# Performance work log

Hardware: AMD Instinct MI355X
Metric: run time of the kernel (lower is better)

## Reference

```python
import jax, jax.numpy as jnp
import numpy as np
from jax import lax

K = 8192
D = 256
BETA = 0.1
DECAY = 0.99
EPS = 1e-05


def setup_inputs() -> dict:
    key = jax.random.key(0)
    k1, k2, k3 = jax.random.split(key, 3)
    z_e = jax.random.normal(k1, (8, 2048, D), dtype=jnp.float32)
    codebook = jax.random.normal(k2, (K, D), dtype=jnp.float32)
    ema_cluster_size = jnp.zeros((K,), dtype=jnp.float32)
    ema_w = jax.random.normal(k3, (K, D), dtype=jnp.float32)
    return {"z_e": z_e, "codebook": codebook,
            "ema_cluster_size": ema_cluster_size, "ema_w": ema_w}


def reference(z_e, codebook, ema_cluster_size, ema_w):
    B, L, Dd = z_e.shape
    # squared-distance matrix (B, L, K): ||z||^2 - 2 z.C^T + ||c||^2
    dist = ((z_e ** 2).sum(-1, keepdims=True)
            - 2.0 * jnp.einsum('bld,kd->blk', z_e, codebook)
            + (codebook ** 2).sum(-1))
    codes = jnp.argmin(dist, axis=-1)          # (B, L) int
    z_q = codebook[codes]                      # gather (B, L, D)

    # training-mode EMA statistics (segment_sum == one_hot.T @ z_e, memory-light)
    flat_codes = codes.reshape(-1)
    flat_z = z_e.reshape(-1, Dd)
    n_i = jax.ops.segment_sum(jnp.ones(flat_codes.shape, dtype=z_e.dtype),
                              flat_codes, num_segments=K)
    dw = jax.ops.segment_sum(flat_z, flat_codes, num_segments=K)
    new_cluster_size = DECAY * ema_cluster_size + (1.0 - DECAY) * n_i
    new_ema_w = DECAY * ema_w + (1.0 - DECAY) * dw
    new_codebook = new_ema_w / (new_cluster_size + EPS)[:, None]

    # straight-through combine and commitment loss
    z_q_st = z_e + lax.stop_gradient(z_q - z_e)
    vq_loss = BETA * jnp.mean((z_e - lax.stop_gradient(z_q)) ** 2)
    return z_q_st, codes, vq_loss, new_codebook, new_cluster_size, new_ema_w
```

## Files before the change

### kernel.cpp

```cpp
#include <hip/hip_runtime.h>
#include <hip/hip_bf16.h>
#include <math.h>

#define N_ROWS 16384
#define DIM    256
#define KCODES 8192

#define OFF_ZQ    0
#define OFF_CODES 4194304
#define OFF_LOSS  4210688
#define OFF_CB    4210689
#define OFF_CS    6307841
#define OFF_EW    6316033
#define OUT_TOTAL 8413185

typedef __attribute__((ext_vector_type(8))) short bf16x8;
typedef __attribute__((ext_vector_type(4))) float f32x4;
typedef __attribute__((ext_vector_type(16))) float f32x16;

__device__ __forceinline__ void gll16(const void* g, void* l) {
  __builtin_amdgcn_global_load_lds(
      (const __attribute__((address_space(1))) unsigned int*)g,
      (__attribute__((address_space(3))) unsigned int*)l, 16, 0, 0);
}

__device__ __forceinline__ unsigned short f2bf(float x) {
  __hip_bfloat16 h = __float2bfloat16(x);
  return *reinterpret_cast<unsigned short*>(&h);
}

__device__ __forceinline__ unsigned umin32(unsigned a, unsigned b) { return a < b ? a : b; }
__device__ __forceinline__ unsigned umax32(unsigned a, unsigned b) { return a > b ? a : b; }

__global__ __launch_bounds__(256) void k_pre(
    const float* __restrict__ z, unsigned short* __restrict__ zbuf,
    const float* __restrict__ cb, unsigned short* __restrict__ cbt,
    float* __restrict__ cnormb, int* __restrict__ cnt,
    float* __restrict__ loss_part) {
  const int b = blockIdx.x;
  const int tid = threadIdx.x;
  if (b < 2048) {
    int i = b * 256 + tid;
    const float4 a = ((const float4*)z)[i * 2];
    const float4 c = ((const float4*)z)[i * 2 + 1];
    union { unsigned short u[8]; uint4 v; } o;
    o.u[0] = f2bf(a.x); o.u[1] = f2bf(a.y); o.u[2] = f2bf(a.z); o.u[3] = f2bf(a.w);
    o.u[4] = f2bf(c.x); o.u[5] = f2bf(c.y); o.u[6] = f2bf(c.z); o.u[7] = f2bf(c.w);
    ((uint4*)zbuf)[i] = o.v;
  } else if (b < 3072) {
    const int code = (b - 2048) * 8 + (tid >> 5);
    const int dq = tid & 31;
    const float4 v0 = *(const float4*)(cb + (size_t)code * 256 + dq * 8);
    const float4 v1 = *(const float4*)(cb + (size_t)code * 256 + dq * 8 + 4);
    union { unsigned short u[8]; uint4 q; } o;
    o.u[0] = f2bf(-2.f * v0.x); o.u[1] = f2bf(-2.f * v0.y);
    o.u[2] = f2bf(-2.f * v0.z); o.u[3] = f2bf(-2.f * v0.w);
    o.u[4] = f2bf(-2.f * v1.x); o.u[5] = f2bf(-2.f * v1.y);
    o.u[6] = f2bf(-2.f * v1.z); o.u[7] = f2bf(-2.f * v1.w);
    *(uint4*)(cbt + ((size_t)dq * 8192 + code) * 8) = o.q;
    float s = v0.x * v0.x + v0.y * v0.y + v0.z * v0.z + v0.w * v0.w +
              v1.x * v1.x + v1.y * v1.y + v1.z * v1.z + v1.w * v1.w;
#pragma unroll
    for (int off = 16; off >= 1; off >>= 1) s += __shfl_down(s, off);
    if ((tid & 31) == 0) cnormb[code] = s + 1024.0f;
  } else if (cnt) {
    int zi = (b - 3072) * 256 + tid;
    if (zi < 8192) cnt[zi] = 0;
    else if (zi < 8448) loss_part[zi - 8192] = 0.0f;
  }
}

__global__ __launch_bounds__(256, 2) void k_argmin(
    const unsigned short* __restrict__ zb,
    const unsigned short* __restrict__ cbt,
    const float* __restrict__ cnb,
    unsigned long long* __restrict__ partials) {
  __shared__ __align__(16) unsigned char lds[73728];

  const int tid = threadIdx.x;
  const int lane = tid & 63;
  const int w = tid >> 6;
  const int wc = w & 1;
  const int wr = w >> 1;
  const int hi = lane >> 5;
  const int l31 = lane & 31;
  const int chunk = blockIdx.x;
  const int r0 = blockIdx.y << 7;

  {
    const char* zgb = (const char*)zb + (size_t)r0 * 512;
#pragma unroll
    for (int it = 0; it < 16; ++it) {
      int s = it * 256 + tid;
      int row = s >> 5;
      int dql = (tid & 31) ^ (row & 31);
      gll16(zgb + row * 512 + dql * 16, lds + s * 16);
    }
    gll16((const char*)cnb + (size_t)chunk * 8192 + tid * 16,
          lds + 65536 + tid * 16);
    gll16((const char*)cnb + (size_t)chunk * 8192 + 4096 + tid * 16,
          lds + 69632 + tid * 16);
  }
  asm volatile("s_waitcnt vmcnt(0)" ::: "memory");
  __builtin_amdgcn_s_barrier();
  __builtin_amdgcn_sched_barrier(0);

  bf16x8 zr0[16], zr1[16];
  {
    const int xr = l31 * 16;
    const int rb0 = (wr * 64 + l31) * 512;
    const int rb1 = (wr * 64 + 32 + l31) * 512;
    const int hx = hi * 16;
#pragma unroll
    for (int ks = 0; ks < 16; ++ks) {
      zr0[ks] = *(const bf16x8*)(lds + rb0 + ((ks * 32 + hx) ^ xr));
      zr1[ks] = *(const bf16x8*)(lds + rb1 + ((ks * 32 + hx) ^ xr));
    }
  }
  asm volatile("s_waitcnt lgkmcnt(0)" ::: "memory");
  __builtin_amdgcn_s_barrier();
  __builtin_amdgcn_sched_barrier(0);

  unsigned char* lcb = lds + tid * 16;
  const char* cgc = (const char*)cbt +
      ((size_t)(tid >> 7) * 131072 + (size_t)chunk * 32768 + (tid & 127) * 16);
  gll16(cgc + 0 * 262144, lcb + 0 * 4096);
  gll16(cgc + 1 * 262144, lcb + 1 * 4096);
  gll16(cgc + 2 * 262144, lcb + 2 * 4096);

  const unsigned char* afp = lds + hi * 2048 + (wc * 64 + l31) * 16;
  const unsigned wchi4 = (unsigned)(wc * 64 + hi * 4);

  unsigned k1_00 = 0xFFFFFFFFu, k2_00 = 0xFFFFFFFFu;
  unsigned k1_01 = 0xFFFFFFFFu, k2_01 = 0xFFFFFFFFu;
  unsigned k1_10 = 0xFFFFFFFFu, k2_10 = 0xFFFFFFFFu;
  unsigned k1_11 = 0xFFFFFFFFu, k2_11 = 0xFFFFFFFFu;
  f32x16 acc00, acc01, acc10, acc11;

#define KSTEP(ks, TAIL)                                                        \
  {                                                                            \
    if ((TAIL) && (ks) == 14) asm volatile("s_waitcnt vmcnt(1)" ::: "memory"); \
    else if ((TAIL) && (ks) == 15) asm volatile("s_waitcnt vmcnt(0)" ::: "memory"); \
    else asm volatile("s_waitcnt vmcnt(2)" ::: "memory");                      \
    __builtin_amdgcn_s_barrier();                                              \
    __builtin_amdgcn_sched_barrier(0);                                         \
    if ((ks) < 13) {                                                           \
      gll16(cgc + ((ks) + 3) * 262144, lcb + (((ks) + 3) & 3) * 4096);         \
    } else if (!(TAIL)) {                                                      \
      gll16(cgc + 2048 + ((ks) - 13) * 262144, lcb + (((ks) + 3) & 3) * 4096); \
    }                                                                          \
    bf16x8 a0 = *(const bf16x8*)(afp + ((ks) & 3) * 4096);                     \
    bf16x8 a1 = *(const bf16x8*)(afp + ((ks) & 3) * 4096 + 512);               \
    acc00 = __builtin_amdgcn_mfma_f32_32x32x16_bf16(a0, zr0[ks], acc00, 0, 0, 0); \
    acc01 = __builtin_amdgcn_mfma_f32_32x32x16_bf16(a0, zr1[ks], acc01, 0, 0, 0); \
    acc10 = __builtin_amdgcn_mfma_f32_32x32x16_bf16(a1, zr0[ks], acc10, 0, 0, 0); \
    acc11 = __builtin_amdgcn_mfma_f32_32x32x16_bf16(a1, zr1[ks], acc11, 0, 0, 0); \
  }

#define MRG(K1V, K2V, KEY)                                                     \
  {                                                                            \
    unsigned t_ = umax32(K1V, (KEY));                                          \
    K2V = umin32(K2V, t_);                                                     \
    K1V = umin32(K1V, (KEY));                                                  \
  }

#define CTBODY(HALF, TAIL)                                                     \
  {                                                                            \
    const int cnoff = 65536 + (HALF) * 4096 + ct * 512 + wc * 256 + hi * 16;   \
    f32x4 cnA[4], cnB[4];                                                      \
    _Pragma("unroll") for (int g2 = 0; g2 < 4; ++g2) {                         \
      cnA[g2] = *(const f32x4*)(lds + cnoff + g2 * 32);                        \
      cnB[g2] = *(const f32x4*)(lds + cnoff + 128 + g2 * 32);                  \
    }                                                                          \
    _Pragma("unroll") for (int r = 0; r < 16; ++r) {                           \
      float vA = cnA[r >> 2][r & 3], vB = cnB[r >> 2][r & 3];                  \
      acc00[r] = vA; acc01[r] = vA; acc10[r] = vB; acc11[r] = vB;              \
    }                                                                          \
    KSTEP(0, TAIL)  KSTEP(1, TAIL)  KSTEP(2, TAIL)  KSTEP(3, TAIL)             \
    KSTEP(4, TAIL)  KSTEP(5, TAIL)  KSTEP(6, TAIL)  KSTEP(7, TAIL)             \
    KSTEP(8, TAIL)  KSTEP(9, TAIL)  KSTEP(10, TAIL) KSTEP(11, TAIL)            \
    KSTEP(12, TAIL) KSTEP(13, TAIL) KSTEP(14, TAIL) KSTEP(15, TAIL)            \
    const unsigned vb = (unsigned)(ct * 128) | wchi4;                          \
    _Pragma("unroll") for (int r = 0; r < 16; ++r) {                           \
      const unsigned base = (unsigned)(8 * (r >> 2) + (r & 3));                \
      unsigned key;                                                            \
      key = (__float_as_uint(acc00[r]) & 0xFFFFFC00u) | (vb | base);           \
      MRG(k1_00, k2_00, key)                                                   \
      key = (__float_as_uint(acc01[r]) & 0xFFFFFC00u) | (vb | base);           \
      MRG(k1_01, k2_01, key)                                                   \
      key = (__float_as_uint(acc10[r]) & 0xFFFFFC00u) | (vb | base | 32u);     \
      MRG(k1_10, k2_10, key)                                                   \
      key = (__float_as_uint(acc11[r]) & 0xFFFFFC00u) | (vb | base | 32u);     \
      MRG(k1_11, k2_11, key)                                                   \
    }                                                                          \
    cgc += 2048;                                                               \
  }

  for (int ct = 0; ct < 8; ++ct) CTBODY(0, false)
  unsigned s1_00 = k1_00, s2_00 = k2_00, s1_01 = k1_01, s2_01 = k2_01;
  unsigned s1_10 = k1_10, s2_10 = k2_10, s1_11 = k1_11, s2_11 = k2_11;
  k1_00 = k2_00 = k1_01 = k2_01 = 0xFFFFFFFFu;
  k1_10 = k2_10 = k1_11 = k2_11 = 0xFFFFFFFFu;

  for (int ct = 0; ct < 7; ++ct) CTBODY(1, false)
  { int ct = 7; CTBODY(1, true) }
#undef CTBODY
#undef MRG
#undef KSTEP

#define FIN(K1V, K2V, ZF, ENT)                                                 \
  {                                                                            \
    unsigned o1 = (unsigned)__shfl_xor((int)(K1V), 32);                        \
    unsigned o2 = (unsigned)__shfl_xor((int)(K2V), 32);                        \
    unsigned n1 = umin32((K1V), o1);                                           \
    unsigned n2 = umin32(umax32((K1V), o1), umin32((K2V), o2));                \
    if (lane < 32) {                                                           \
      int row = r0 + wr * 64 + (ZF) * 32 + l31;                                \
      partials[(size_t)row * 32 + (ENT)] =                                     \
          ((unsigned long long)n2 << 32) | n1;                                 \
    }                                                                          \
  }
  const int eb = chunk * 8 + wc * 2;
  FIN(s1_00, s2_00, 0, eb + 0) FIN(s1_10, s2_10, 0, eb + 1)
  FIN(s1_01, s2_01, 1, eb + 0) FIN(s1_11, s2_11, 1, eb + 1)
  FIN(k1_00, k2_00, 0, eb + 4) FIN(k1_10, k2_10, 0, eb + 5)
  FIN(k1_01, k2_01, 1, eb + 4) FIN(k1_11, k2_11, 1, eb + 5)
#undef FIN
}

__global__ __launch_bounds__(256) void k_reduce(
    const unsigned long long* __restrict__ partials, const float* __restrict__ z,
    const float* __restrict__ cb, float* __restrict__ out_codes,
    int* __restrict__ cnt, float* __restrict__ zq,
    float* __restrict__ loss_part) {
  const int row = blockIdx.x * 4 + (threadIdx.x >> 6);
  const int lane = threadIdx.x & 63;
  const int e = lane & 31;

  unsigned myK1 = 0xFFFFFFFFu, myK2 = 0xFFFFFFFFu;
  if (lane < 32) {
    unsigned long long v = partials[(size_t)row * 32 + e];
    myK1 = (unsigned)v; myK2 = (unsigned)(v >> 32);
  }
  unsigned K1 = myK1, K2 = myK2;
  int bc = e >> 2;
#pragma unroll
  for (int m = 1; m <= 32; m <<= 1) {
    unsigned o1 = (unsigned)__shfl_xor((int)K1, m);
    unsigned o2 = (unsigned)__shfl_xor((int)K2, m);
    int ob = __shfl_xor(bc, m);
    unsigned nK2 = umin32(umax32(K1, o1), umin32(K2, o2));
    if (o1 < K1 || (o1 == K1 && ob < bc)) { K1 = o1; bc = ob; }
    K2 = nK2;
  }
  int chosen = bc * 1024 + (int)(K1 & 1023u);

  const float* zr = z + ((size_t)row << 8);
  float r1 = __uint_as_float(K1 & 0xFFFFFC00u);
  float r2 = __uint_as_float(K2 & 0xFFFFFC00u);
  if (r2 - r1 < 0.75f) {
    const float win = r1 + 0.75f;
    double bestd = 1e300; int bestj = 0x7fffffff;
#pragma unroll
    for (int h = 0; h < 2; ++h) {
      unsigned k = h ? myK2 : myK1;
      float bv = __uint_as_float(k & 0xFFFFFC00u);
      if (lane < 32 && bv <= win) {
        int jv = (e >> 2) * 1024 + (int)(k & 1023u);
        const float* c = cb + ((size_t)jv << 8);
        double d = 0.0;
        for (int kk = 0; kk < DIM; ++kk) {
          double df = (double)zr[kk] - (double)c[kk];
          d += df * df;
        }
        if (d < bestd || (d == bestd && jv < bestj)) { bestd = d; bestj = jv; }
      }
    }
#pragma unroll
    for (int m = 1; m <= 32; m <<= 1) {
      double od = __shfl_xor(bestd, m);
      int oj = __shfl_xor(bestj, m);
      if (od < bestd || (od == bestd && oj < bestj)) { bestd = od; bestj = oj; }
    }
    chosen = bestj;
  }
  if (lane == 0) {
    out_codes[row] = (float)chosen;
    if (cnt) atomicAdd(&cnt[chosen], 1);
  }

  if (zq) {
    const float* cq = cb + ((size_t)chosen << 8);
    float4 zv = ((const float4*)zr)[lane];
    float4 qv = ((const float4*)cq)[lane];
    ((float4*)(zq + ((size_t)row << 8)))[lane] = qv;
    float d0 = zv.x - qv.x, d1 = zv.y - qv.y;
    float d2 = zv.z - qv.z, d3 = zv.w - qv.w;
    float lacc = (d0 * d0 + d1 * d1) + (d2 * d2 + d3 * d3);
#pragma unroll
    for (int off = 32; off >= 1; off >>= 1) lacc += __shfl_down(lacc, off);
    __shared__ float wls[4];
    if (lane == 0) wls[threadIdx.x >> 6] = lacc;
    __syncthreads();
    if (threadIdx.x == 0) {
      float s = (wls[0] + wls[1]) + (wls[2] + wls[3]);
      atomicAdd(loss_part + (blockIdx.x & 255), s * (float)(0.1 / 4194304.0));
    }
  }
}

__global__ __launch_bounds__(1024) void k_scanplace(
    const int* __restrict__ cnt, int* __restrict__ start,
    const float* __restrict__ ema_cs, float* __restrict__ cs_out,
    const float* __restrict__ codesf, int* __restrict__ rowlist) {
  __shared__ int lcur[8192];
  __shared__ int wsum[16], wbase[16];
  const int t = threadIdx.x;
  const int lane = t & 63, wid = t >> 6;
  const int base = t * 8;
  int c[8], s = 0;
#pragma unroll
  for (int i = 0; i < 8; ++i) { c[i] = cnt[base + i]; s += c[i]; }
  int inc = s;
#pragma unroll
  for (int off = 1; off < 64; off <<= 1) {
    int v = __shfl_up(inc, off);
    if (lane >= off) inc += v;
  }
  if (lane == 63) wsum[wid] = inc;
  __syncthreads();
  if (t < 16) {
    int v = wsum[t];
    int winc = v;
#pragma unroll
    for (int off = 1; off < 16; off <<= 1) {
      int u = __shfl_up(winc, off);
      if (t >= off) winc += u;
    }
    wbase[t] = winc - v;
  }
  __syncthreads();
  int ex = wbase[wid] + (inc - s);
#pragma unroll
  for (int i = 0; i < 8; ++i) {
    start[base + i] = ex;
    lcur[base + i] = ex;
    cs_out[base + i] = 0.99f * ema_cs[base + i] + 0.01f * (float)c[i];
    ex += c[i];
  }
  __syncthreads();
#pragma unroll
  for (int rr = 0; rr < 16; ++rr) {
    int r = rr * 1024 + t;
    int cc = (int)codesf[r];
    int p = atomicAdd(&lcur[cc], 1);
    rowlist[p] = r;
  }
}

__global__ __launch_bounds__(256) void k_dw2(
    const float* __restrict__ z, const int* __restrict__ start,
    const int* __restrict__ cnt, const int* __restrict__ rowlist,
    const float* __restrict__ ema_w, const float* __restrict__ cs_new,
    float* __restrict__ ew, float* __restrict__ cb_out) {
  const int k = blockIdx.x;
  const int d = threadIdx.x;
  const int s = start[k], n = cnt[k];
  const size_t o = ((size_t)k << 8) + d;
  float a0 = 0.f, a1 = 0.f, a2 = 0.f, a3 = 0.f;
  int t = 0;
  for (; t + 4 <= n; t += 4) {
    size_t ro0 = ((size_t)rowlist[s + t] << 8) + d;
    size_t ro1 = ((size_t)rowlist[s + t + 1] << 8) + d;
    size_t ro2 = ((size_t)rowlist[s + t + 2] << 8) + d;
    size_t ro3 = ((size_t)rowlist[s + t + 3] << 8) + d;
    a0 += z[ro0]; a1 += z[ro1]; a2 += z[ro2]; a3 += z[ro3];
  }
  for (; t < n; ++t)
    a0 += z[((size_t)rowlist[s + t] << 8) + d];
  float a = (a0 + a1) + (a2 + a3);
  const float v = 0.99f * ema_w[o] + 0.01f * a;
  ew[o] = v;
  cb_out[o] = v / (cs_new[k] + 1e-5f);
}

__global__ __launch_bounds__(256) void k_loss_final(
    const float* __restrict__ part, float* __restrict__ loss) {
  float s = part[threadIdx.x];
#pragma unroll
  for (int off = 32; off >= 1; off >>= 1) s += __shfl_down(s, off);
  __shared__ float w[4];
  if ((threadIdx.x & 63) == 0) w[threadIdx.x >> 6] = s;
  __syncthreads();
  if (threadIdx.x == 0) loss[0] = (w[0] + w[1]) + (w[2] + w[3]);
}

__global__ __launch_bounds__(256) void k_scatter(
    const float* __restrict__ z, const float* __restrict__ cb,
    const float* __restrict__ codesf, float* __restrict__ zq,
    float* __restrict__ loss, float* __restrict__ cs_acc,
    float* __restrict__ ew_acc) {
  const int row = blockIdx.x;
  const int d = threadIdx.x;
  const int c = (int)codesf[row];
  const float zv = z[((size_t)row << 8) + d];
  const float qv = cb[((size_t)c << 8) + d];
  zq[((size_t)row << 8) + d] = zv + (qv - zv);
  float diff = zv - qv;
  float sq = diff * diff;
#pragma unroll
  for (int off = 32; off >= 1; off >>= 1) sq += __shfl_down(sq, off);
  __shared__ float wpart[4];
  if ((d & 63) == 0) wpart[d >> 6] = sq;
  __syncthreads();
  if (d == 0) {
    float s = (wpart[0] + wpart[1]) + (wpart[2] + wpart[3]);
    atomicAdd(loss, s * (float)(0.1 / 4194304.0));
    atomicAdd(cs_acc + c, 1.0f);
  }
  atomicAdd(ew_acc + ((size_t)c << 8) + d, zv);
}

__global__ __launch_bounds__(256) void k_ema_cs(const float* __restrict__ ema_cs,
                                                float* __restrict__ cs_io) {
  const int k = blockIdx.x * 256 + threadIdx.x;
  const float cnt = cs_io[k];
  cs_io[k] = 0.99f * ema_cs[k] + 0.01f * cnt;
}

__global__ __launch_bounds__(256) void k_ema_w(const float* __restrict__ ema_w,
                                               const float* __restrict__ cs_new,
                                               float* __restrict__ ew_io,
                                               float* __restrict__ cb_out) {
  const int i = blockIdx.x * 256 + threadIdx.x;
  const float dw = ew_io[i];
  const float v = 0.99f * ema_w[i] + 0.01f * dw;
  ew_io[i] = v;
  cb_out[i] = v / (cs_new[i >> 8] + 1e-5f);
}

extern "C" void kernel_launch(void* const* d_in, const int* in_sizes, int n_in,
                              void* d_out, int out_size, void* d_ws, size_t ws_size,
                              hipStream_t stream) {
  const float* z      = (const float*)d_in[0];
  const float* cb     = (const float*)d_in[1];
  const float* ema_cs = (const float*)d_in[2];
  const float* ema_w  = (const float*)d_in[3];
  float* out = (float*)d_out;

  float* o_zq    = out + OFF_ZQ;
  float* o_codes = out + OFF_CODES;
  float* o_loss  = out + OFF_LOSS;
  float* o_cb    = out + OFF_CB;
  float* o_cs    = out + OFF_CS;
  float* o_ew    = out + OFF_EW;

  uintptr_t zb_a  = ((uintptr_t)o_cb + 15) & ~(uintptr_t)15;
  uintptr_t cbt_a = ((uintptr_t)o_ew + 15) & ~(uintptr_t)15;
  unsigned short* zbuf = (unsigned short*)zb_a;
  unsigned short* cbt  = (unsigned short*)cbt_a;

  const size_t ws_need = 4 * (8192 * 2 + 16384 + 256 + 8192);
  const bool sorted = (ws_size >= ws_need);
  int* cnt      = (int*)d_ws;
  int* start    = cnt + 8192;
  int* rowlist  = start + 8192;
  float* loss_part = (float*)(rowlist + 16384);
  float* cnorm_ws  = loss_part + 256;

  float* cnorm;
  unsigned long long* partials;
  if (sorted) {
    cnorm    = cnorm_ws;
    partials = (unsigned long long*)(cbt_a + 4194304);
  } else {
    cnorm    = (float*)(cbt_a + 4194304);
    partials = (unsigned long long*)o_zq;
  }

  k_pre<<<3105, 256, 0, stream>>>(z, zbuf, cb, cbt, cnorm,
                                  sorted ? cnt : (int*)nullptr, loss_part);

  dim3 g(4, 128);
  k_argmin<<<g, 256, 0, stream>>>(zbuf, cbt, cnorm, partials);
  k_reduce<<<N_ROWS / 4, 256, 0, stream>>>(
      partials, z, cb, o_codes, sorted ? cnt : (int*)nullptr,
      sorted ? o_zq : (float*)nullptr, loss_part);

  if (sorted) {
    k_scanplace<<<1, 1024, 0, stream>>>(cnt, start, ema_cs, o_cs, o_codes,
                                        rowlist);
    k_dw2<<<KCODES, 256, 0, stream>>>(z, start, cnt, rowlist, ema_w, o_cs,
                                      o_ew, o_cb);
    k_loss_final<<<1, 256, 0, stream>>>(loss_part, o_loss);
  } else {
    (void)hipMemsetAsync(o_loss, 0,
                         (size_t)(OUT_TOTAL - OFF_LOSS) * sizeof(float), stream);
    k_scatter<<<N_ROWS, 256, 0, stream>>>(z, cb, o_codes, o_zq, o_loss, o_cs,
                                          o_ew);
    k_ema_cs<<<KCODES / 256, 256, 0, stream>>>(ema_cs, o_cs);
    k_ema_w <<<KCODES * DIM / 256, 256, 0, stream>>>(ema_w, o_cs, o_ew, o_cb);
  }
}
```

Measured before the change: 156.2 us.

## Deepen argmin LDS prefetch to six stages and split scan/place kernels

The argmin GEMM loop now keeps six global-to-LDS codebook loads in flight across an 8-slot ring and runs two k-steps per barrier, where before it kept three loads in flight across 4 slots with one barrier per step. This halves the barriers and hides more memory latency, at the cost of more LDS. Separately, the single-block scan+placement kernel is split into a scan kernel plus a 64-block placement kernel using global atomics on a cursor array. This spreads the row-list scatter across many CUs but adds a launch, and row order within each bucket may differ.

```diff
diff --git a/kernel.cpp b/kernel.cpp
--- a/kernel.cpp
+++ b/kernel.cpp
@@ -124,9 +124,9 @@
   unsigned char* lcb = lds + tid * 16;
   const char* cgc = (const char*)cbt +
       ((size_t)(tid >> 7) * 131072 + (size_t)chunk * 32768 + (tid & 127) * 16);
-  gll16(cgc + 0 * 262144, lcb + 0 * 4096);
-  gll16(cgc + 1 * 262144, lcb + 1 * 4096);
-  gll16(cgc + 2 * 262144, lcb + 2 * 4096);
+#pragma unroll
+  for (int s = 0; s < 6; ++s)
+    gll16(cgc + s * 262144, lcb + s * 4096);
 
   const unsigned char* afp = lds + hi * 2048 + (wc * 64 + l31) * 16;
   const unsigned wchi4 = (unsigned)(wc * 64 + hi * 4);
@@ -137,24 +137,34 @@
   unsigned k1_11 = 0xFFFFFFFFu, k2_11 = 0xFFFFFFFFu;
   f32x16 acc00, acc01, acc10, acc11;
 
-#define KSTEP(ks, TAIL)                                                        \
+#define PAIR(pp, TAIL)                                                         \
   {                                                                            \
-    if ((TAIL) && (ks) == 14) asm volatile("s_waitcnt vmcnt(1)" ::: "memory"); \
-    else if ((TAIL) && (ks) == 15) asm volatile("s_waitcnt vmcnt(0)" ::: "memory"); \
-    else asm volatile("s_waitcnt vmcnt(2)" ::: "memory");                      \
+    if ((TAIL) && (pp) == 6) asm volatile("s_waitcnt vmcnt(2)" ::: "memory");  \
+    else if ((TAIL) && (pp) == 7) asm volatile("s_waitcnt vmcnt(0)" ::: "memory"); \
+    else asm volatile("s_waitcnt vmcnt(4)" ::: "memory");                      \
     __builtin_amdgcn_s_barrier();                                              \
     __builtin_amdgcn_sched_barrier(0);                                         \
-    if ((ks) < 13) {                                                           \
-      gll16(cgc + ((ks) + 3) * 262144, lcb + (((ks) + 3) & 3) * 4096);         \
-    } else if (!(TAIL)) {                                                      \
-      gll16(cgc + 2048 + ((ks) - 13) * 262144, lcb + (((ks) + 3) & 3) * 4096); \
+    if (!(TAIL) || (pp) < 5) {          \
+      const int s0_ = 2 * (pp) + 6, s1_ = 2 * (pp) + 7;                        \
+      gll16(cgc + ((s0_ < 16) ? s0_ * 262144 : 2048 + (s0_ - 16) * 262144),    \
+            lcb + (s0_ & 7) * 4096);                                           \
+      gll16(cgc + ((s1_ < 16) ? s1_ * 262144 : 2048 + (s1_ - 16) * 262144),    \
+            lcb + (s1_ & 7) * 4096);                                           \
     }                                                                          \
-    bf16x8 a0 = *(const bf16x8*)(afp + ((ks) & 3) * 4096);                     \
-    bf16x8 a1 = *(const bf16x8*)(afp + ((ks) & 3) * 4096 + 512);               \
-    acc00 = __builtin_amdgcn_mfma_f32_32x32x16_bf16(a0, zr0[ks], acc00, 0, 0, 0); \
-    acc01 = __builtin_amdgcn_mfma_f32_32x32x16_bf16(a0, zr1[ks], acc01, 0, 0, 0); \
-    acc10 = __builtin_amdgcn_mfma_f32_32x32x16_bf16(a1, zr0[ks], acc10, 0, 0, 0); \
-    acc11 = __builtin_amdgcn_mfma_f32_32x32x16_bf16(a1, zr1[ks], acc11, 0, 0, 0); \
+    {                                                                          \
+      bf16x8 a0 = *(const bf16x8*)(afp + ((2 * (pp)) & 7) * 4096);             \
+      bf16x8 b0 = *(const bf16x8*)(afp + ((2 * (pp)) & 7) * 4096 + 512);       \
+      acc00 = __builtin_amdgcn_mfma_f32_32x32x16_bf16(a0, zr0[2 * (pp)], acc00, 0, 0, 0); \
+      acc01 = __builtin_amdgcn_mfma_f32_32x32x16_bf16(a0, zr1[2 * (pp)], acc01, 0, 0, 0); \
+      acc10 = __builtin_amdgcn_mfma_f32_32x32x16_bf16(b0, zr0[2 * (pp)], acc10, 0, 0, 0); \
+      acc11 = __builtin_amdgcn_mfma_f32_32x32x16_bf16(b0, zr1[2 * (pp)], acc11, 0, 0, 0); \
+      bf16x8 a1 = *(const bf16x8*)(afp + ((2 * (pp) + 1) & 7) * 4096);         \
+      bf16x8 b1 = *(const bf16x8*)(afp + ((2 * (pp) + 1) & 7) * 4096 + 512);   \
+      acc00 = __builtin_amdgcn_mfma_f32_32x32x16_bf16(a1, zr0[2 * (pp) + 1], acc00, 0, 0, 0); \
+      acc01 = __builtin_amdgcn_mfma_f32_32x32x16_bf16(a1, zr1[2 * (pp) + 1], acc01, 0, 0, 0); \
+      acc10 = __builtin_amdgcn_mfma_f32_32x32x16_bf16(b1, zr0[2 * (pp) + 1], acc10, 0, 0, 0); \
+      acc11 = __builtin_amdgcn_mfma_f32_32x32x16_bf16(b1, zr1[2 * (pp) + 1], acc11, 0, 0, 0); \
+    }                                                                          \
   }
 
 #define MRG(K1V, K2V, KEY)                                                     \
@@ -176,10 +186,8 @@
       float vA = cnA[r >> 2][r & 3], vB = cnB[r >> 2][r & 3];                  \
       acc00[r] = vA; acc01[r] = vA; acc10[r] = vB; acc11[r] = vB;              \
     }                                                                          \
-    KSTEP(0, TAIL)  KSTEP(1, TAIL)  KSTEP(2, TAIL)  KSTEP(3, TAIL)             \
-    KSTEP(4, TAIL)  KSTEP(5, TAIL)  KSTEP(6, TAIL)  KSTEP(7, TAIL)             \
-    KSTEP(8, TAIL)  KSTEP(9, TAIL)  KSTEP(10, TAIL) KSTEP(11, TAIL)            \
-    KSTEP(12, TAIL) KSTEP(13, TAIL) KSTEP(14, TAIL) KSTEP(15, TAIL)            \
+    PAIR(0, TAIL) PAIR(1, TAIL) PAIR(2, TAIL) PAIR(3, TAIL)                    \
+    PAIR(4, TAIL) PAIR(5, TAIL) PAIR(6, TAIL) PAIR(7, TAIL)                    \
     const unsigned vb = (unsigned)(ct * 128) | wchi4;                          \
     _Pragma("unroll") for (int r = 0; r < 16; ++r) {                           \
       const unsigned base = (unsigned)(8 * (r >> 2) + (r & 3));                \
@@ -206,7 +214,7 @@
   { int ct = 7; CTBODY(1, true) }
 #undef CTBODY
 #undef MRG
-#undef KSTEP
+#undef PAIR
 
 #define FIN(K1V, K2V, ZF, ENT)                                                 \
   {                                                                            \
@@ -309,11 +317,10 @@
   }
 }
 
-__global__ __launch_bounds__(1024) void k_scanplace(
+__global__ __launch_bounds__(1024) void k_scan(
     const int* __restrict__ cnt, int* __restrict__ start,
-    const float* __restrict__ ema_cs, float* __restrict__ cs_out,
-    const float* __restrict__ codesf, int* __restrict__ rowlist) {
-  __shared__ int lcur[8192];
+    int* __restrict__ cursor, const float* __restrict__ ema_cs,
+    float* __restrict__ cs_out) {
   __shared__ int wsum[16], wbase[16];
   const int t = threadIdx.x;
   const int lane = t & 63, wid = t >> 6;
@@ -344,18 +351,19 @@
 #pragma unroll
   for (int i = 0; i < 8; ++i) {
     start[base + i] = ex;
-    lcur[base + i] = ex;
+    cursor[base + i] = ex;
     cs_out[base + i] = 0.99f * ema_cs[base + i] + 0.01f * (float)c[i];
     ex += c[i];
   }
-  __syncthreads();
-#pragma unroll
-  for (int rr = 0; rr < 16; ++rr) {
-    int r = rr * 1024 + t;
-    int cc = (int)codesf[r];
-    int p = atomicAdd(&lcur[cc], 1);
-    rowlist[p] = r;
-  }
+}
+
+__global__ __launch_bounds__(256) void k_place(const float* __restrict__ codesf,
+                                               int* __restrict__ cursor,
+                                               int* __restrict__ rowlist) {
+  int i = blockIdx.x * 256 + threadIdx.x;
+  int c = (int)codesf[i];
+  int p = atomicAdd(&cursor[c], 1);
+  rowlist[p] = i;
 }
 
 __global__ __launch_bounds__(256) void k_dw2(
@@ -488,8 +496,9 @@
       sorted ? o_zq : (float*)nullptr, loss_part);
 
   if (sorted) {
-    k_scanplace<<<1, 1024, 0, stream>>>(cnt, start, ema_cs, o_cs, o_codes,
-                                        rowlist);
+    int* cursor = (int*)cnorm_ws;
+    k_scan <<<1, 1024, 0, stream>>>(cnt, start, cursor, ema_cs, o_cs);
+    k_place<<<64, 256, 0, stream>>>(o_codes, cursor, rowlist);
     k_dw2<<<KCODES, 256, 0, stream>>>(z, start, cnt, rowlist, ema_w, o_cs,
                                       o_ew, o_cb);
     k_loss_final<<<1, 256, 0, stream>>>(loss_part, o_loss);
```

Measured after the change: 148.4 us. -5.0%, faster.
